# Optimization experiments

Measured on AMD Instinct MI355X. Metric: run time of the kernel, lower is better.

## Reference

```python
import jax, jax.numpy as jnp
import numpy as np

N = 50000      # num nodes
E = 800000     # num directed edges (before self loops)
C_IN = 128     # input channels
HID = 128      # hidden channels per head
H = 2          # attention heads (layer 0)
NEG_SLOPE = 0.2


def setup_inputs() -> dict:
    key = jax.random.key(0)
    ks = jax.random.split(key, 10)
    s = 0.05
    return {
        "x": jax.random.normal(ks[0], (N, C_IN), jnp.float32),
        "edge_index": jax.random.randint(ks[1], (2, E), 0, N, dtype=jnp.int32),
        "W1": jax.random.normal(ks[2], (C_IN, H * HID), jnp.float32) * s,
        "att_src1": jax.random.normal(ks[3], (H, HID), jnp.float32) * s,
        "att_dst1": jax.random.normal(ks[4], (H, HID), jnp.float32) * s,
        "b1": jax.random.normal(ks[5], (H * HID,), jnp.float32) * s,
        "W2": jax.random.normal(ks[6], (H * HID, 1), jnp.float32) * s,
        "att_src2": jax.random.normal(ks[7], (1, 1), jnp.float32) * s,
        "att_dst2": jax.random.normal(ks[8], (1, 1), jnp.float32) * s,
        "b2": jax.random.normal(ks[9], (1,), jnp.float32) * s,
    }


def gat_layer(x, src, dst, W, att_src, att_dst, bias, heads, out_ch, concat, num_nodes):
    # linear projection -> [N, H, C]
    h = (x @ W).reshape(num_nodes, heads, out_ch)
    a_src = jnp.einsum("nhc,hc->nh", h, att_src)  # [N, H]
    a_dst = jnp.einsum("nhc,hc->nh", h, att_dst)  # [N, H]
    # edge attention logits, LeakyReLU as in GATConv
    alpha = jax.nn.leaky_relu(a_src[src] + a_dst[dst], NEG_SLOPE)  # [Etot, H]
    # segment softmax over incoming edges of each destination node
    amax = jax.ops.segment_max(alpha, dst, num_segments=num_nodes)
    amax = jnp.where(jnp.isfinite(amax), amax, 0.0)
    ex = jnp.exp(alpha - amax[dst])
    denom = jax.ops.segment_sum(ex, dst, num_segments=num_nodes)
    coef = ex / (denom[dst] + 1e-16)                      # [Etot, H]
    # weighted scatter-aggregate of source features
    msg = h[src] * coef[:, :, None]                       # [Etot, H, C]
    out = jax.ops.segment_sum(msg, dst, num_segments=num_nodes)  # [N, H, C]
    out = out.reshape(num_nodes, heads * out_ch) if concat else out.mean(axis=1)
    return out + bias


def reference(x, edge_index, W1, att_src1, att_dst1, b1, W2, att_src2, att_dst2, b2):
    n = x.shape[0]
    loops = jnp.arange(n, dtype=edge_index.dtype)
    src = jnp.concatenate([edge_index[0], loops])  # GATConv adds self-loops
    dst = jnp.concatenate([edge_index[1], loops])
    h = gat_layer(x, src, dst, W1, att_src1, att_dst1, b1, H, HID, True, n)
    h = jax.nn.relu(h)
    out = gat_layer(h, src, dst, W2, att_src2, att_dst2, b2, 1, 1, False, n)
    return jax.nn.sigmoid(out)  # [N, 1]
```

## Files before the change

kernel.cpp:

```cpp
#include <hip/hip_runtime.h>
#include <hip/hip_bf16.h>

#define NEG_SLOPE 0.2f

using bf16x8 = __attribute__((ext_vector_type(8))) short;
using f32x4  = __attribute__((ext_vector_type(4))) float;

__device__ inline unsigned short f2bf(float f) {
  __hip_bfloat16 b = __float2bfloat16(f);
  return __builtin_bit_cast(unsigned short, b);
}
__device__ inline float bf2f(unsigned short u) {
  return __uint_as_float(((unsigned)u) << 16);
}

__global__ __launch_bounds__(256) void k0_w1t(
    const float* __restrict__ W1, unsigned short* __restrict__ W1T) {
  const int e = blockIdx.x * 256 + threadIdx.x;
  const int k = e >> 8, c = e & 255;
  W1T[c * 128 + k] = f2bf(W1[e]);
}

__global__ __launch_bounds__(256) void k1_mfma(
    const float* __restrict__ x, const unsigned short* __restrict__ W1T,
    const float* __restrict__ att_src, const float* __restrict__ att_dst,
    unsigned short* __restrict__ h1bf, float4* __restrict__ attn, int N) {
  __shared__ short xs[64][136];
  const int t = threadIdx.x;
  const int w = t >> 6, l = t & 63;
  const int n0 = blockIdx.x * 64;

  {
    const int col4 = (t & 31) * 4;
#pragma unroll
    for (int p = 0; p < 8; ++p) {
      const int row = p * 8 + (t >> 5);
      float4 xv = make_float4(0.f, 0.f, 0.f, 0.f);
      if (n0 + row < N) xv = *(const float4*)(x + (size_t)(n0 + row) * 128 + col4);
      ushort4 u;
      u.x = f2bf(xv.x); u.y = f2bf(xv.y); u.z = f2bf(xv.z); u.w = f2bf(xv.w);
      *(ushort4*)&xs[row][col4] = u;
    }
  }
  __syncthreads();

  f32x4 acc[16];
#pragma unroll
  for (int nf = 0; nf < 16; ++nf) acc[nf] = f32x4{0.f, 0.f, 0.f, 0.f};
  const int cb = l & 15;
  const int ar = w * 16 + cb;
  const int kof = (l >> 4) * 8;
#pragma unroll
  for (int kk = 0; kk < 4; ++kk) {
    const bf16x8 a = *(const bf16x8*)&xs[ar][kk * 32 + kof];
#pragma unroll
    for (int nf = 0; nf < 16; ++nf) {
      const bf16x8 b = *(const bf16x8*)(W1T + (size_t)(nf * 16 + cb) * 128 + kk * 32 + kof);
      acc[nf] = __builtin_amdgcn_mfma_f32_16x16x32_bf16(a, b, acc[nf], 0, 0, 0);
    }
  }

  const int rbase = n0 + w * 16 + (l >> 4) * 4;

#pragma unroll
  for (int r = 0; r < 4; ++r) {
    const int node = rbase + r;
    if (node < N) {
#pragma unroll
      for (int nf = 0; nf < 16; ++nf)
        h1bf[(size_t)node * 256 + nf * 16 + cb] = f2bf(acc[nf][r]);
    }
  }

  float av[16], dv[16];
#pragma unroll
  for (int nf = 0; nf < 16; ++nf) {
    av[nf] = att_src[nf * 16 + cb];
    dv[nf] = att_dst[nf * 16 + cb];
  }
#pragma unroll
  for (int r = 0; r < 4; ++r) {
    float ps0 = 0.f, ps1 = 0.f, pd0 = 0.f, pd1 = 0.f;
#pragma unroll
    for (int nf = 0; nf < 8; ++nf) {
      ps0 = fmaf(acc[nf][r], av[nf], ps0);
      pd0 = fmaf(acc[nf][r], dv[nf], pd0);
    }
#pragma unroll
    for (int nf = 8; nf < 16; ++nf) {
      ps1 = fmaf(acc[nf][r], av[nf], ps1);
      pd1 = fmaf(acc[nf][r], dv[nf], pd1);
    }
    for (int m = 1; m < 16; m <<= 1) {
      ps0 += __shfl_xor(ps0, m);
      ps1 += __shfl_xor(ps1, m);
      pd0 += __shfl_xor(pd0, m);
      pd1 += __shfl_xor(pd1, m);
    }
    const int node = rbase + r;
    if (cb == 0 && node < N) attn[node] = make_float4(ps0, ps1, pd0, pd1);
  }
}

__global__ __launch_bounds__(256) void k_deg(
    const int* __restrict__ ei, int E, int Etot,
    int* __restrict__ deg, int* __restrict__ off) {
  const int e = blockIdx.x * 256 + threadIdx.x;
  if (e >= Etot) return;
  const int d = (e < E) ? ei[E + e] : (e - E);
  off[e] = atomicAdd(&deg[d], 1);
}

#define SCH 196

__global__ __launch_bounds__(256) void k_scanA(
    const int* __restrict__ deg, int* __restrict__ bsum, int N) {
  const int b = blockIdx.x, t = threadIdx.x;
  const int i = b * SCH + t;
  int v = (t < SCH && i < N) ? deg[i] : 0;
  for (int m = 32; m; m >>= 1) v += __shfl_xor(v, m);
  __shared__ int ps[4];
  if ((t & 63) == 0) ps[t >> 6] = v;
  __syncthreads();
  if (t == 0) bsum[b] = ps[0] + ps[1] + ps[2] + ps[3];
}

__global__ __launch_bounds__(256) void k_scanBC(
    const int* __restrict__ deg, const int* __restrict__ bsum,
    int* __restrict__ rowptr, int N, int Etot) {
  __shared__ int sc[256];
  __shared__ int ownoff;
  const int b = blockIdx.x, t = threadIdx.x;
  const int v = bsum[t];
  sc[t] = v;
  __syncthreads();
  for (int off = 1; off < 256; off <<= 1) {
    const int u = (t >= off) ? sc[t - off] : 0;
    __syncthreads();
    sc[t] += u;
    __syncthreads();
  }
  if (t == b) ownoff = sc[t] - v;
  __syncthreads();
  const int i = b * SCH + t;
  const int d = (t < SCH && i < N) ? deg[i] : 0;
  sc[t] = d;
  __syncthreads();
  for (int off = 1; off < 256; off <<= 1) {
    const int u = (t >= off) ? sc[t - off] : 0;
    __syncthreads();
    sc[t] += u;
    __syncthreads();
  }
  if (t < SCH && i < N) rowptr[i] = ownoff + sc[t] - d;
  if (b == 0 && t == 0) rowptr[N] = Etot;
}

__global__ __launch_bounds__(256) void k_scatter(
    const int* __restrict__ ei, int E, int Etot,
    const int* __restrict__ rowptr, const int* __restrict__ off,
    const float4* __restrict__ attn, int4* __restrict__ rec) {
  const int e = blockIdx.x * 256 + threadIdx.x;
  if (e >= Etot) return;
  int s, d;
  if (e < E) { s = ei[e]; d = ei[E + e]; } else { s = e - E; d = s; }
  const int pos = rowptr[d] + off[e];
  const float4 as = attn[s];
  const float4 ad = attn[d];
  float a0 = as.x + ad.z;
  float a1 = as.y + ad.w;
  a0 = a0 > 0.f ? a0 : a0 * NEG_SLOPE;
  a1 = a1 > 0.f ? a1 : a1 * NEG_SLOPE;
  int4 r;
  r.x = s;
  r.y = __float_as_int(__expf(a0));
  r.z = __float_as_int(__expf(a1));
  r.w = 0;
  rec[pos] = r;
}

__global__ __launch_bounds__(256) void k3_gather(
    const int* __restrict__ rowptr, const int4* __restrict__ rec,
    const unsigned short* __restrict__ h1bf,
    const float* __restrict__ b1, const float* __restrict__ W2,
    float* __restrict__ h2, int N) {
  const int wave = threadIdx.x >> 6, lane = threadIdx.x & 63;
  const int n = blockIdx.x * 4 + wave;
  if (n >= N) return;
  const bool hi = lane >= 32;
  const int beg = rowptr[n], end = rowptr[n + 1];
  float4 acc = {0.f, 0.f, 0.f, 0.f};
  float den = 0.f;

  for (int base = beg; base < end; base += 64) {
    const int m = end - base;
    int sv = 0;
    float wx = 0.f, wy = 0.f;
    if (lane < m) {
      const int4 rv = rec[base + lane];
      sv = rv.x;
      wx = __int_as_float(rv.y);
      wy = __int_as_float(rv.z);
    }
    const int kcnt = m < 64 ? m : 64;

    int s0 = __shfl(sv, 0), s1 = __shfl(sv, 1), s2 = __shfl(sv, 2), s3 = __shfl(sv, 3);
    ushort4 h0 = ((const ushort4*)(h1bf + (size_t)s0 * 256))[lane];
    ushort4 h1 = ((const ushort4*)(h1bf + (size_t)s1 * 256))[lane];
    ushort4 h2v = ((const ushort4*)(h1bf + (size_t)s2 * 256))[lane];
    ushort4 h3 = ((const ushort4*)(h1bf + (size_t)s3 * 256))[lane];

    for (int i = 0; i < kcnt; i += 4) {
      const int j0 = (i + 4) & 63, j1 = (i + 5) & 63, j2 = (i + 6) & 63, j3 = (i + 7) & 63;
      const int t0 = __shfl(sv, j0), t1 = __shfl(sv, j1), t2 = __shfl(sv, j2), t3 = __shfl(sv, j3);
      const ushort4 g0 = ((const ushort4*)(h1bf + (size_t)t0 * 256))[lane];
      const ushort4 g1 = ((const ushort4*)(h1bf + (size_t)t1 * 256))[lane];
      const ushort4 g2 = ((const ushort4*)(h1bf + (size_t)t2 * 256))[lane];
      const ushort4 g3 = ((const ushort4*)(h1bf + (size_t)t3 * 256))[lane];

      const float wxa = __shfl(wx, i),     wya = __shfl(wy, i);
      const float wxb = __shfl(wx, i + 1), wyb = __shfl(wy, i + 1);
      const float wxc = __shfl(wx, i + 2), wyc = __shfl(wy, i + 2);
      const float wxd = __shfl(wx, i + 3), wyd = __shfl(wy, i + 3);
      const float w0 = hi ? wya : wxa;
      const float w1 = hi ? wyb : wxb;
      const float w2 = hi ? wyc : wxc;
      const float w3 = hi ? wyd : wxd;

      acc.x = fmaf(bf2f(h0.x), w0, acc.x); acc.y = fmaf(bf2f(h0.y), w0, acc.y);
      acc.z = fmaf(bf2f(h0.z), w0, acc.z); acc.w = fmaf(bf2f(h0.w), w0, acc.w);
      acc.x = fmaf(bf2f(h1.x), w1, acc.x); acc.y = fmaf(bf2f(h1.y), w1, acc.y);
      acc.z = fmaf(bf2f(h1.z), w1, acc.z); acc.w = fmaf(bf2f(h1.w), w1, acc.w);
      acc.x = fmaf(bf2f(h2v.x), w2, acc.x); acc.y = fmaf(bf2f(h2v.y), w2, acc.y);
      acc.z = fmaf(bf2f(h2v.z), w2, acc.z); acc.w = fmaf(bf2f(h2v.w), w2, acc.w);
      acc.x = fmaf(bf2f(h3.x), w3, acc.x); acc.y = fmaf(bf2f(h3.y), w3, acc.y);
      acc.z = fmaf(bf2f(h3.z), w3, acc.z); acc.w = fmaf(bf2f(h3.w), w3, acc.w);
      den += w0 + w1 + w2 + w3;

      h0 = g0; h1 = g1; h2v = g2; h3 = g3;
    }
  }

  const float inv = 1.f / (den + 1e-16f);
  const float4 bv = ((const float4*)b1)[lane];
  const float4 wv4 = ((const float4*)W2)[lane];
  float p = 0.f;
  p += fmaxf(fmaf(acc.x, inv, bv.x), 0.f) * wv4.x;
  p += fmaxf(fmaf(acc.y, inv, bv.y), 0.f) * wv4.y;
  p += fmaxf(fmaf(acc.z, inv, bv.z), 0.f) * wv4.z;
  p += fmaxf(fmaf(acc.w, inv, bv.w), 0.f) * wv4.w;
  for (int m = 32; m; m >>= 1) p += __shfl_xor(p, m);
  if (lane == 0) h2[n] = p;
}

__global__ __launch_bounds__(256) void k_l2(
    const int* __restrict__ rowptr, const int4* __restrict__ rec,
    const float* __restrict__ h2,
    const float* __restrict__ att_s2, const float* __restrict__ att_d2,
    const float* __restrict__ b2, float* __restrict__ out, int N) {
  const int wave = threadIdx.x >> 6, lane = threadIdx.x & 63;
  const int n = blockIdx.x * 4 + wave;
  if (n >= N) return;
  const float as2 = att_s2[0];
  const float hd = h2[n] * att_d2[0];
  const int beg = rowptr[n], end = rowptr[n + 1];
  float num = 0.f, den = 0.f;
  for (int base = beg; base < end; base += 64) {
    if (base + lane < end) {
      const float hs = h2[rec[base + lane].x];
      float a = fmaf(hs, as2, hd);
      a = a > 0.f ? a : a * NEG_SLOPE;
      const float w = __expf(a);
      den += w;
      num = fmaf(w, hs, num);
    }
  }
  for (int m = 32; m; m >>= 1) { num += __shfl_xor(num, m); den += __shfl_xor(den, m); }
  if (lane == 0) {
    const float v = num / (den + 1e-16f) + b2[0];
    out[n] = 1.f / (1.f + __expf(-v));
  }
}

extern "C" void kernel_launch(void* const* d_in, const int* in_sizes, int n_in,
                              void* d_out, int out_size, void* d_ws, size_t ws_size,
                              hipStream_t stream) {
  const float* x        = (const float*)d_in[0];
  const int*   ei       = (const int*)d_in[1];
  const float* W1       = (const float*)d_in[2];
  const float* att_src1 = (const float*)d_in[3];
  const float* att_dst1 = (const float*)d_in[4];
  const float* b1       = (const float*)d_in[5];
  const float* W2       = (const float*)d_in[6];
  const float* att_s2   = (const float*)d_in[7];
  const float* att_d2   = (const float*)d_in[8];
  const float* b2       = (const float*)d_in[9];
  float* out = (float*)d_out;

  const int N = in_sizes[0] / 128;
  const int E = in_sizes[1] / 2;
  const int Etot = E + N;

  char* ws = (char*)d_ws;
  size_t o = 0;
  unsigned short* h1bf = (unsigned short*)(ws + o); o += (size_t)N * 256 * 2;
  float4* attn = (float4*)(ws + o); o += (size_t)N * 16;
  int4* rec    = (int4*)(ws + o); o += (size_t)Etot * 16;
  unsigned short* W1T  = (unsigned short*)(ws + o); o += (size_t)256 * 128 * 2;
  float* h2  = (float*)(ws + o); o += (size_t)N * 4;
  int* rowptr = (int*)(ws + o); o += (size_t)(N + 1) * 4 + 4;
  int* off    = (int*)(ws + o); o += (size_t)Etot * 4;
  int* bsum   = (int*)(ws + o); o += 256 * 4;
  const size_t zoff = o;
  int* deg = (int*)(ws + o); o += (size_t)N * 4;

  hipMemsetAsync(ws + zoff, 0, o - zoff, stream);

  k0_w1t<<<128, 256, 0, stream>>>(W1, W1T);
  k1_mfma<<<(N + 63) / 64, 256, 0, stream>>>(x, W1T, att_src1, att_dst1, h1bf, attn, N);
  k_deg<<<(Etot + 255) / 256, 256, 0, stream>>>(ei, E, Etot, deg, off);
  k_scanA<<<256, 256, 0, stream>>>(deg, bsum, N);
  k_scanBC<<<256, 256, 0, stream>>>(deg, bsum, rowptr, N, Etot);
  k_scatter<<<(Etot + 255) / 256, 256, 0, stream>>>(ei, E, Etot, rowptr, off, attn, rec);
  k3_gather<<<(N + 3) / 4, 256, 0, stream>>>(rowptr, rec, h1bf, b1, W2, h2, N);
  k_l2<<<(N + 3) / 4, 256, 0, stream>>>(rowptr, rec, h2, att_s2, att_d2, b2, out, N);
}
```

Baseline: 259.9 us.

## Switch to fp16 MFMA, pack edge records, fuse init kernels, narrow layer-2 groups

Projected features now use fp16 instead of bf16. The MFMA operands are swapped so each lane holds four consecutive channels of one node, which allows vectorized ushort4 stores and a shorter attention-logit reduction. Edge records shrink from 16 to 8 bytes by packing the two exp weights as bf16, which cuts scatter writes and gather reads. The W1 transpose and degree-count kernels are merged into one launch. Layer 2 now gives each node 16 lanes instead of a full wave, since average degree is about 17. The risks are fp16 range and precision on the features and bf16 rounding on the attention weights.

```diff
diff --git a/kernel.cpp b/kernel.cpp
--- a/kernel.cpp
+++ b/kernel.cpp
@@ -3,29 +3,43 @@
 
 #define NEG_SLOPE 0.2f
 
-using bf16x8 = __attribute__((ext_vector_type(8))) short;
-using f32x4  = __attribute__((ext_vector_type(4))) float;
+using f16x8 = __attribute__((ext_vector_type(8))) _Float16;
+using f32x4 = __attribute__((ext_vector_type(4))) float;
 
 __device__ inline unsigned short f2bf(float f) {
   __hip_bfloat16 b = __float2bfloat16(f);
   return __builtin_bit_cast(unsigned short, b);
 }
-__device__ inline float bf2f(unsigned short u) {
-  return __uint_as_float(((unsigned)u) << 16);
-}
-
-__global__ __launch_bounds__(256) void k0_w1t(
-    const float* __restrict__ W1, unsigned short* __restrict__ W1T) {
-  const int e = blockIdx.x * 256 + threadIdx.x;
-  const int k = e >> 8, c = e & 255;
-  W1T[c * 128 + k] = f2bf(W1[e]);
+__device__ inline unsigned short f2h(float f) {
+  return __builtin_bit_cast(unsigned short, (_Float16)f);
+}
+__device__ inline float h2f(unsigned short u) {
+  return (float)__builtin_bit_cast(_Float16, u);
+}
+
+__global__ __launch_bounds__(256) void k_init(
+    const float* __restrict__ W1, _Float16* __restrict__ W1T,
+    const int* __restrict__ ei, int E, int Etot,
+    int* __restrict__ deg, int* __restrict__ off) {
+  const int b = blockIdx.x, t = threadIdx.x;
+  if (b < 128) {
+    const int e = b * 256 + t;
+    const int k = e >> 8, c = e & 255;
+    W1T[c * 128 + k] = (_Float16)W1[e];
+  } else {
+    const int e = (b - 128) * 256 + t;
+    if (e < Etot) {
+      const int d = (e < E) ? ei[E + e] : (e - E);
+      off[e] = atomicAdd(&deg[d], 1);
+    }
+  }
 }
 
 __global__ __launch_bounds__(256) void k1_mfma(
-    const float* __restrict__ x, const unsigned short* __restrict__ W1T,
+    const float* __restrict__ x, const _Float16* __restrict__ W1T,
     const float* __restrict__ att_src, const float* __restrict__ att_dst,
-    unsigned short* __restrict__ h1bf, float4* __restrict__ attn, int N) {
-  __shared__ short xs[64][136];
+    _Float16* __restrict__ h1f, float4* __restrict__ attn, int N) {
+  __shared__ _Float16 xs[64][136];
   const int t = threadIdx.x;
   const int w = t >> 6, l = t & 63;
   const int n0 = blockIdx.x * 64;
@@ -38,7 +52,7 @@
       float4 xv = make_float4(0.f, 0.f, 0.f, 0.f);
       if (n0 + row < N) xv = *(const float4*)(x + (size_t)(n0 + row) * 128 + col4);
       ushort4 u;
-      u.x = f2bf(xv.x); u.y = f2bf(xv.y); u.z = f2bf(xv.z); u.w = f2bf(xv.w);
+      u.x = f2h(xv.x); u.y = f2h(xv.y); u.z = f2h(xv.z); u.w = f2h(xv.w);
       *(ushort4*)&xs[row][col4] = u;
     }
   }
@@ -48,67 +62,44 @@
 #pragma unroll
   for (int nf = 0; nf < 16; ++nf) acc[nf] = f32x4{0.f, 0.f, 0.f, 0.f};
   const int cb = l & 15;
-  const int ar = w * 16 + cb;
   const int kof = (l >> 4) * 8;
+  const int xr = w * 16 + cb;
 #pragma unroll
   for (int kk = 0; kk < 4; ++kk) {
-    const bf16x8 a = *(const bf16x8*)&xs[ar][kk * 32 + kof];
+    const f16x8 bx = *(const f16x8*)&xs[xr][kk * 32 + kof];
 #pragma unroll
     for (int nf = 0; nf < 16; ++nf) {
-      const bf16x8 b = *(const bf16x8*)(W1T + (size_t)(nf * 16 + cb) * 128 + kk * 32 + kof);
-      acc[nf] = __builtin_amdgcn_mfma_f32_16x16x32_bf16(a, b, acc[nf], 0, 0, 0);
-    }
-  }
-
-  const int rbase = n0 + w * 16 + (l >> 4) * 4;
-
-#pragma unroll
-  for (int r = 0; r < 4; ++r) {
-    const int node = rbase + r;
-    if (node < N) {
-#pragma unroll
-      for (int nf = 0; nf < 16; ++nf)
-        h1bf[(size_t)node * 256 + nf * 16 + cb] = f2bf(acc[nf][r]);
-    }
-  }
-
-  float av[16], dv[16];
+      const f16x8 aw = *(const f16x8*)(W1T + (size_t)(nf * 16 + cb) * 128 + kk * 32 + kof);
+      acc[nf] = __builtin_amdgcn_mfma_f32_16x16x32_f16(aw, bx, acc[nf], 0, 0, 0);
+    }
+  }
+
+  const int node = n0 + w * 16 + cb;
+  const int cg = (l >> 4) * 4;
+  if (node < N) {
+#pragma unroll
+    for (int nf = 0; nf < 16; ++nf) {
+      ushort4 u;
+      u.x = f2h(acc[nf][0]); u.y = f2h(acc[nf][1]);
+      u.z = f2h(acc[nf][2]); u.w = f2h(acc[nf][3]);
+      *(ushort4*)(h1f + (size_t)node * 256 + nf * 16 + cg) = u;
+    }
+  }
+
+  float s0 = 0.f, s1 = 0.f, d0 = 0.f, d1 = 0.f;
 #pragma unroll
   for (int nf = 0; nf < 16; ++nf) {
-    av[nf] = att_src[nf * 16 + cb];
-    dv[nf] = att_dst[nf * 16 + cb];
-  }
-#pragma unroll
-  for (int r = 0; r < 4; ++r) {
-    float ps0 = 0.f, ps1 = 0.f, pd0 = 0.f, pd1 = 0.f;
-#pragma unroll
-    for (int nf = 0; nf < 8; ++nf) {
-      ps0 = fmaf(acc[nf][r], av[nf], ps0);
-      pd0 = fmaf(acc[nf][r], dv[nf], pd0);
-    }
-#pragma unroll
-    for (int nf = 8; nf < 16; ++nf) {
-      ps1 = fmaf(acc[nf][r], av[nf], ps1);
-      pd1 = fmaf(acc[nf][r], dv[nf], pd1);
-    }
-    for (int m = 1; m < 16; m <<= 1) {
-      ps0 += __shfl_xor(ps0, m);
-      ps1 += __shfl_xor(ps1, m);
-      pd0 += __shfl_xor(pd0, m);
-      pd1 += __shfl_xor(pd1, m);
-    }
-    const int node = rbase + r;
-    if (cb == 0 && node < N) attn[node] = make_float4(ps0, ps1, pd0, pd1);
-  }
-}
-
-__global__ __launch_bounds__(256) void k_deg(
-    const int* __restrict__ ei, int E, int Etot,
-    int* __restrict__ deg, int* __restrict__ off) {
-  const int e = blockIdx.x * 256 + threadIdx.x;
-  if (e >= Etot) return;
-  const int d = (e < E) ? ei[E + e] : (e - E);
-  off[e] = atomicAdd(&deg[d], 1);
+    const float4 av = *(const float4*)(att_src + nf * 16 + cg);
+    const float4 dv = *(const float4*)(att_dst + nf * 16 + cg);
+    const float ls = acc[nf][0] * av.x + acc[nf][1] * av.y + acc[nf][2] * av.z + acc[nf][3] * av.w;
+    const float ld = acc[nf][0] * dv.x + acc[nf][1] * dv.y + acc[nf][2] * dv.z + acc[nf][3] * dv.w;
+    if (nf < 8) { s0 += ls; d0 += ld; } else { s1 += ls; d1 += ld; }
+  }
+  s0 += __shfl_xor(s0, 16); s0 += __shfl_xor(s0, 32);
+  s1 += __shfl_xor(s1, 16); s1 += __shfl_xor(s1, 32);
+  d0 += __shfl_xor(d0, 16); d0 += __shfl_xor(d0, 32);
+  d1 += __shfl_xor(d1, 16); d1 += __shfl_xor(d1, 32);
+  if (l < 16 && node < N) attn[node] = make_float4(s0, s1, d0, d1);
 }
 
 #define SCH 196
@@ -159,7 +150,7 @@
 __global__ __launch_bounds__(256) void k_scatter(
     const int* __restrict__ ei, int E, int Etot,
     const int* __restrict__ rowptr, const int* __restrict__ off,
-    const float4* __restrict__ attn, int4* __restrict__ rec) {
+    const float4* __restrict__ attn, int2* __restrict__ rec) {
   const int e = blockIdx.x * 256 + threadIdx.x;
   if (e >= Etot) return;
   int s, d;
@@ -171,17 +162,13 @@
   float a1 = as.y + ad.w;
   a0 = a0 > 0.f ? a0 : a0 * NEG_SLOPE;
   a1 = a1 > 0.f ? a1 : a1 * NEG_SLOPE;
-  int4 r;
-  r.x = s;
-  r.y = __float_as_int(__expf(a0));
-  r.z = __float_as_int(__expf(a1));
-  r.w = 0;
-  rec[pos] = r;
+  const unsigned int wp = ((unsigned)f2bf(__expf(a1)) << 16) | f2bf(__expf(a0));
+  rec[pos] = make_int2(s, (int)wp);
 }
 
 __global__ __launch_bounds__(256) void k3_gather(
-    const int* __restrict__ rowptr, const int4* __restrict__ rec,
-    const unsigned short* __restrict__ h1bf,
+    const int* __restrict__ rowptr, const int2* __restrict__ rec,
+    const _Float16* __restrict__ h1f,
     const float* __restrict__ b1, const float* __restrict__ W2,
     float* __restrict__ h2, int N) {
   const int wave = threadIdx.x >> 6, lane = threadIdx.x & 63;
@@ -191,50 +178,49 @@
   const int beg = rowptr[n], end = rowptr[n + 1];
   float4 acc = {0.f, 0.f, 0.f, 0.f};
   float den = 0.f;
+  const unsigned short* h1u = (const unsigned short*)h1f;
 
   for (int base = beg; base < end; base += 64) {
     const int m = end - base;
-    int sv = 0;
-    float wx = 0.f, wy = 0.f;
+    int sv = 0, wp = 0;
     if (lane < m) {
-      const int4 rv = rec[base + lane];
+      const int2 rv = rec[base + lane];
       sv = rv.x;
-      wx = __int_as_float(rv.y);
-      wy = __int_as_float(rv.z);
+      wp = rv.y;
     }
     const int kcnt = m < 64 ? m : 64;
 
-    int s0 = __shfl(sv, 0), s1 = __shfl(sv, 1), s2 = __shfl(sv, 2), s3 = __shfl(sv, 3);
-    ushort4 h0 = ((const ushort4*)(h1bf + (size_t)s0 * 256))[lane];
-    ushort4 h1 = ((const ushort4*)(h1bf + (size_t)s1 * 256))[lane];
-    ushort4 h2v = ((const ushort4*)(h1bf + (size_t)s2 * 256))[lane];
-    ushort4 h3 = ((const ushort4*)(h1bf + (size_t)s3 * 256))[lane];
+    int s0_ = __shfl(sv, 0), s1_ = __shfl(sv, 1), s2_ = __shfl(sv, 2), s3_ = __shfl(sv, 3);
+    ushort4 h0 = ((const ushort4*)(h1u + (size_t)s0_ * 256))[lane];
+    ushort4 h1 = ((const ushort4*)(h1u + (size_t)s1_ * 256))[lane];
+    ushort4 h2v = ((const ushort4*)(h1u + (size_t)s2_ * 256))[lane];
+    ushort4 h3 = ((const ushort4*)(h1u + (size_t)s3_ * 256))[lane];
 
     for (int i = 0; i < kcnt; i += 4) {
       const int j0 = (i + 4) & 63, j1 = (i + 5) & 63, j2 = (i + 6) & 63, j3 = (i + 7) & 63;
       const int t0 = __shfl(sv, j0), t1 = __shfl(sv, j1), t2 = __shfl(sv, j2), t3 = __shfl(sv, j3);
-      const ushort4 g0 = ((const ushort4*)(h1bf + (size_t)t0 * 256))[lane];
-      const ushort4 g1 = ((const ushort4*)(h1bf + (size_t)t1 * 256))[lane];
-      const ushort4 g2 = ((const ushort4*)(h1bf + (size_t)t2 * 256))[lane];
-      const ushort4 g3 = ((const ushort4*)(h1bf + (size_t)t3 * 256))[lane];
-
-      const float wxa = __shfl(wx, i),     wya = __shfl(wy, i);
-      const float wxb = __shfl(wx, i + 1), wyb = __shfl(wy, i + 1);
-      const float wxc = __shfl(wx, i + 2), wyc = __shfl(wy, i + 2);
-      const float wxd = __shfl(wx, i + 3), wyd = __shfl(wy, i + 3);
-      const float w0 = hi ? wya : wxa;
-      const float w1 = hi ? wyb : wxb;
-      const float w2 = hi ? wyc : wxc;
-      const float w3 = hi ? wyd : wxd;
-
-      acc.x = fmaf(bf2f(h0.x), w0, acc.x); acc.y = fmaf(bf2f(h0.y), w0, acc.y);
-      acc.z = fmaf(bf2f(h0.z), w0, acc.z); acc.w = fmaf(bf2f(h0.w), w0, acc.w);
-      acc.x = fmaf(bf2f(h1.x), w1, acc.x); acc.y = fmaf(bf2f(h1.y), w1, acc.y);
-      acc.z = fmaf(bf2f(h1.z), w1, acc.z); acc.w = fmaf(bf2f(h1.w), w1, acc.w);
-      acc.x = fmaf(bf2f(h2v.x), w2, acc.x); acc.y = fmaf(bf2f(h2v.y), w2, acc.y);
-      acc.z = fmaf(bf2f(h2v.z), w2, acc.z); acc.w = fmaf(bf2f(h2v.w), w2, acc.w);
-      acc.x = fmaf(bf2f(h3.x), w3, acc.x); acc.y = fmaf(bf2f(h3.y), w3, acc.y);
-      acc.z = fmaf(bf2f(h3.z), w3, acc.z); acc.w = fmaf(bf2f(h3.w), w3, acc.w);
+      const ushort4 g0 = ((const ushort4*)(h1u + (size_t)t0 * 256))[lane];
+      const ushort4 g1 = ((const ushort4*)(h1u + (size_t)t1 * 256))[lane];
+      const ushort4 g2 = ((const ushort4*)(h1u + (size_t)t2 * 256))[lane];
+      const ushort4 g3 = ((const ushort4*)(h1u + (size_t)t3 * 256))[lane];
+
+      const unsigned int wp0 = (unsigned)__shfl(wp, i);
+      const unsigned int wp1 = (unsigned)__shfl(wp, i + 1);
+      const unsigned int wp2 = (unsigned)__shfl(wp, i + 2);
+      const unsigned int wp3 = (unsigned)__shfl(wp, i + 3);
+      const float w0 = __uint_as_float(hi ? (wp0 & 0xffff0000u) : (wp0 << 16));
+      const float w1 = __uint_as_float(hi ? (wp1 & 0xffff0000u) : (wp1 << 16));
+      const float w2 = __uint_as_float(hi ? (wp2 & 0xffff0000u) : (wp2 << 16));
+      const float w3 = __uint_as_float(hi ? (wp3 & 0xffff0000u) : (wp3 << 16));
+
+      acc.x = fmaf(h2f(h0.x), w0, acc.x); acc.y = fmaf(h2f(h0.y), w0, acc.y);
+      acc.z = fmaf(h2f(h0.z), w0, acc.z); acc.w = fmaf(h2f(h0.w), w0, acc.w);
+      acc.x = fmaf(h2f(h1.x), w1, acc.x); acc.y = fmaf(h2f(h1.y), w1, acc.y);
+      acc.z = fmaf(h2f(h1.z), w1, acc.z); acc.w = fmaf(h2f(h1.w), w1, acc.w);
+      acc.x = fmaf(h2f(h2v.x), w2, acc.x); acc.y = fmaf(h2f(h2v.y), w2, acc.y);
+      acc.z = fmaf(h2f(h2v.z), w2, acc.z); acc.w = fmaf(h2f(h2v.w), w2, acc.w);
+      acc.x = fmaf(h2f(h3.x), w3, acc.x); acc.y = fmaf(h2f(h3.y), w3, acc.y);
+      acc.z = fmaf(h2f(h3.z), w3, acc.z); acc.w = fmaf(h2f(h3.w), w3, acc.w);
       den += w0 + w1 + w2 + w3;
 
       h0 = g0; h1 = g1; h2v = g2; h3 = g3;
@@ -254,20 +240,20 @@
 }
 
 __global__ __launch_bounds__(256) void k_l2(
-    const int* __restrict__ rowptr, const int4* __restrict__ rec,
+    const int* __restrict__ rowptr, const int2* __restrict__ rec,
     const float* __restrict__ h2,
     const float* __restrict__ att_s2, const float* __restrict__ att_d2,
     const float* __restrict__ b2, float* __restrict__ out, int N) {
-  const int wave = threadIdx.x >> 6, lane = threadIdx.x & 63;
-  const int n = blockIdx.x * 4 + wave;
+  const int sub = threadIdx.x & 15;
+  const int n = blockIdx.x * 16 + (threadIdx.x >> 4);
   if (n >= N) return;
   const float as2 = att_s2[0];
   const float hd = h2[n] * att_d2[0];
   const int beg = rowptr[n], end = rowptr[n + 1];
   float num = 0.f, den = 0.f;
-  for (int base = beg; base < end; base += 64) {
-    if (base + lane < end) {
-      const float hs = h2[rec[base + lane].x];
+  for (int base = beg; base < end; base += 16) {
+    if (base + sub < end) {
+      const float hs = h2[rec[base + sub].x];
       float a = fmaf(hs, as2, hd);
       a = a > 0.f ? a : a * NEG_SLOPE;
       const float w = __expf(a);
@@ -275,8 +261,8 @@
       num = fmaf(w, hs, num);
     }
   }
-  for (int m = 32; m; m >>= 1) { num += __shfl_xor(num, m); den += __shfl_xor(den, m); }
-  if (lane == 0) {
+  for (int m = 8; m; m >>= 1) { num += __shfl_xor(num, m); den += __shfl_xor(den, m); }
+  if (sub == 0) {
     const float v = num / (den + 1e-16f) + b2[0];
     out[n] = 1.f / (1.f + __expf(-v));
   }
@@ -303,10 +289,10 @@
 
   char* ws = (char*)d_ws;
   size_t o = 0;
-  unsigned short* h1bf = (unsigned short*)(ws + o); o += (size_t)N * 256 * 2;
   float4* attn = (float4*)(ws + o); o += (size_t)N * 16;
-  int4* rec    = (int4*)(ws + o); o += (size_t)Etot * 16;
-  unsigned short* W1T  = (unsigned short*)(ws + o); o += (size_t)256 * 128 * 2;
+  int2* rec    = (int2*)(ws + o); o += (size_t)Etot * 8;
+  _Float16* h1f = (_Float16*)(ws + o); o += (size_t)N * 256 * 2;
+  _Float16* W1T = (_Float16*)(ws + o); o += (size_t)256 * 128 * 2;
   float* h2  = (float*)(ws + o); o += (size_t)N * 4;
   int* rowptr = (int*)(ws + o); o += (size_t)(N + 1) * 4 + 4;
   int* off    = (int*)(ws + o); o += (size_t)Etot * 4;
@@ -316,12 +302,11 @@
 
   hipMemsetAsync(ws + zoff, 0, o - zoff, stream);
 
-  k0_w1t<<<128, 256, 0, stream>>>(W1, W1T);
-  k1_mfma<<<(N + 63) / 64, 256, 0, stream>>>(x, W1T, att_src1, att_dst1, h1bf, attn, N);
-  k_deg<<<(Etot + 255) / 256, 256, 0, stream>>>(ei, E, Etot, deg, off);
+  k_init<<<128 + (Etot + 255) / 256, 256, 0, stream>>>(W1, W1T, ei, E, Etot, deg, off);
+  k1_mfma<<<(N + 63) / 64, 256, 0, stream>>>(x, W1T, att_src1, att_dst1, h1f, attn, N);
   k_scanA<<<256, 256, 0, stream>>>(deg, bsum, N);
   k_scanBC<<<256, 256, 0, stream>>>(deg, bsum, rowptr, N, Etot);
   k_scatter<<<(Etot + 255) / 256, 256, 0, stream>>>(ei, E, Etot, rowptr, off, attn, rec);
-  k3_gather<<<(N + 3) / 4, 256, 0, stream>>>(rowptr, rec, h1bf, b1, W2, h2, N);
-  k_l2<<<(N + 3) / 4, 256, 0, stream>>>(rowptr, rec, h2, att_s2, att_d2, b2, out, N);
-}
+  k3_gather<<<(N + 3) / 4, 256, 0, stream>>>(rowptr, rec, h1f, b1, W2, h2, N);
+  k_l2<<<(N + 15) / 16, 256, 0, stream>>>(rowptr, rec, h2, att_s2, att_d2, b2, out, N);
+}
```

Result: no change. 255.2 us (-1.8%).
